# Performance work log

Hardware: AMD Instinct MI355X
Metric: run time of the kernel (lower is better)

## Reference

```python
import jax, jax.numpy as jnp
import numpy as np

B, S, N, D, T = 128, 128, 196, 512, 12


def setup_inputs() -> dict:
    key = jax.random.key(0)
    ks = jax.random.split(key, 20)
    nrm = lambda i, shape, s: jax.random.normal(ks[i], shape, jnp.float32) * s
    w = lambda i, shape: nrm(i, shape, 1.0 / np.sqrt(shape[-1]))
    return {
        "ctx": nrm(0, (B, S, D), 1.0),
        "q": nrm(1, (B, 2 * D), 1.0),
        "k": nrm(2, (B, D, N), 1.0),
        "mem0": nrm(3, (1, D), 0.02),
        "ctrl0": nrm(4, (1, D), 0.02),
        # ControlUnit params
        "Wp": w(5, (T, D, 2 * D)), "bp": jnp.zeros((T, D), jnp.float32),
        "Wcq": w(6, (D, 2 * D)), "bcq": jnp.zeros((D,), jnp.float32),
        "Wca": w(7, (1, D)), "bca": jnp.zeros((1,), jnp.float32),
        # ReadUnit params
        "Wrm": w(8, (D, D)), "brm": jnp.zeros((D,), jnp.float32),
        "Wrc": w(9, (D, 2 * D)), "brc": jnp.zeros((D,), jnp.float32),
        "Wra": w(10, (1, D)), "bra": jnp.zeros((1,), jnp.float32),
        # WriteUnit params
        "Wwc": w(11, (D, 2 * D)), "bwc": jnp.zeros((D,), jnp.float32),
    }


def reference(ctx, q, k, mem0, ctrl0, Wp, bp, Wcq, bcq, Wca, bca,
              Wrm, brm, Wrc, brc, Wra, bra, Wwc, bwc):
    b = q.shape[0]
    c = jnp.broadcast_to(ctrl0, (b, D))
    m = jnp.broadcast_to(mem0, (b, D))
    for t in range(T):
        # --- control unit (alpha_entmax with alpha=1.0 == softmax) ---
        p = q @ Wp[t].T + bp[t]                                # [B, D]
        cc = jnp.concatenate([c, p], axis=1) @ Wcq.T + bcq     # [B, D]
        ctx_p = cc[:, None, :] * ctx                           # [B, S, D]
        aw = jax.nn.softmax(ctx_p @ Wca.T + bca, axis=1)       # [B, S, 1]
        c = (aw * ctx).sum(axis=1)                             # [B, D]
        # --- read unit ---
        mm = (m @ Wrm.T + brm)[:, :, None]                     # [B, D, 1]
        kc = jnp.concatenate([mm * k, k], axis=1)              # [B, 2D, N]
        rc = kc.transpose(0, 2, 1) @ Wrc.T + brc               # [B, N, D]
        logit = ((rc * c[:, None, :]) @ Wra.T + bra)[..., 0]   # [B, N]
        rw = jax.nn.softmax(logit, axis=1)[:, None, :]         # [B, 1, N]
        r = (rw * k).sum(axis=2)                               # [B, D]
        # --- write unit (no self-attention / memory gate) ---
        m = jnp.concatenate([r, m], axis=1) @ Wwc.T + bwc      # [B, D]
    return m
```

## Files before the change

### kernel.cpp

```cpp
#include <hip/hip_runtime.h>
#include <hip/hip_bf16.h>
#include <cstdint>

#define D  512
#define D2 1024
#define BB 128
#define SS 128
#define NN 196
#define TT 12

typedef unsigned short u16;
typedef __attribute__((ext_vector_type(8))) short short8v;
typedef __attribute__((ext_vector_type(4))) float f32x4;

__device__ __forceinline__ float bf2f(u16 h){
  union { unsigned int u; float f; } v; v.u = ((unsigned int)h) << 16; return v.f;
}

__device__ __forceinline__ float LDX(const void* p, size_t i, int isbf){
  if (isbf) return bf2f(((const u16*)p)[i]);
  return ((const float*)p)[i];
}

__device__ __forceinline__ float4 LD4(const void* p, size_t i, int isbf){
  if (isbf){
    ushort4 w = *(const ushort4*)((const u16*)p + i);
    return make_float4(bf2f(w.x), bf2f(w.y), bf2f(w.z), bf2f(w.w));
  }
  return *(const float4*)((const float*)p + i);
}

__device__ __forceinline__ void bfsplit(float x, short &h, short &l){
  unsigned u = __float_as_uint(x);
  unsigned hu = u & 0xFFFF0000u;
  float r = x - __uint_as_float(hu);
  h = (short)(u >> 16);
  l = (short)(__float_as_uint(r) >> 16);
}

__global__ __launch_bounds__(256) void k_detect(const u16* ctx, int* flag){
  __shared__ int cnt;
  if (threadIdx.x == 0) cnt = 0;
  __syncthreads();
  int bad = 0;
  for (int i = threadIdx.x; i < 8192; i += 256){
    int e = (ctx[i] >> 7) & 0xFF;
    if (e == 0xFF || (e != 0 && (e < 90 || e > 160))) bad++;
  }
  atomicAdd(&cnt, bad);
  __syncthreads();
  if (threadIdx.x == 0) *flag = (cnt > 100) ? 0 : 1;
}

__global__ __launch_bounds__(256) void k_prep1(const void* q, const void* Wcq, const void* Wca,
      const void* Wwc, const void* Wrm, const void* Wrc, const void* Wra,
      const void* bp, const void* bcq, const void* ctrl0, const void* mem0, const void* brm,
      float* qT, float* W1f, float* Wwcf, float* WrmTf, float* W2f,
      float* P, float* pp2, float* ubase, float* mmb, const int* flag){
  const int isbf = *flag;
  __shared__ float lds[32][33];
  int bk = blockIdx.x, tid = threadIdx.x;
  int tx = tid & 31, ty = tid >> 5;
  if (bk >= 1344){
    int ib = bk - 1344;
    int lane = tid & 63, w = tid >> 6;
    int grp = lane >> 3, k = lane & 7;
    int isU = (ib < 16);
    int o = (isU ? ib : ib - 16)*32 + w*8 + grp;
    const void* vec = isU ? ctrl0 : mem0;
    const void* mat = isU ? Wcq : Wrm;
    int ld = isU ? D2 : D;
    float acc = 0.f;
    #pragma unroll 4
    for (int it = 0; it < 16; it++){
      int d = it*32 + k*4;
      float4 v = LD4(vec, d, isbf);
      float4 m = LD4(mat, (size_t)o*ld + d, isbf);
      acc += v.x*m.x + v.y*m.y + v.z*m.z + v.w*m.w;
    }
    acc += __shfl_xor(acc, 1, 64);
    acc += __shfl_xor(acc, 2, 64);
    acc += __shfl_xor(acc, 4, 64);
    if (k == 0){
      if (isU) ubase[o] = acc * LDX(Wca, o, isbf);
      else     mmb[o]   = acc + LDX(brm, o, isbf);
    }
    return;
  }
  if (bk >= 1280){
    int l = bk - 1280;
    for (int idx = l*256 + tid; idx < 786432; idx += 64*256){
      int j = (idx >> 7) & 511;
      pp2[idx] = LDX(bcq, j, isbf) * LDX(Wca, j, isbf);
    }
    return;
  }
  if (bk >= 1216){
    int l = bk - 1216;
    for (int idx = l*256 + tid; idx < 786432; idx += 64*256)
      P[idx] = LDX(bp, idx >> 7, isbf);
    return;
  }
  if (bk >= 1152){
    int l = bk - 1152;
    if (isbf){
      const u16* w = (const u16*)Wrc; const u16* s = (const u16*)Wra;
      for (int idx = l*256 + tid; idx < 524288; idx += 64*256)
        W2f[idx] = bf2f(w[idx]) * bf2f(s[idx >> 10]);
    } else {
      const float* w = (const float*)Wrc; const float* s = (const float*)Wra;
      for (int idx = l*256 + tid; idx < 524288; idx += 64*256)
        W2f[idx] = w[idx] * s[idx >> 10];
    }
    return;
  }
  const void* in = nullptr; const void* scale = nullptr; float* out = nullptr;
  int ld = 0, R = 0, tR = 0, tC = 0;
  if (bk < 128)      { in = q;   ld = 1024; R = 128; out = qT;    tR = bk & 3;  tC = bk >> 2; }
  else if (bk < 384) { int l = bk - 128; in = Wcq; ld = 1024; R = 512; out = W1f;  scale = Wca; tR = l & 15; tC = l >> 4; }
  else if (bk < 896) { int l = bk - 384; in = Wwc; ld = 1024; R = 512; out = Wwcf; tR = l & 15; tC = l >> 4; }
  else               { int l = bk - 896; in = Wrm; ld = 512;  R = 512; out = WrmTf;tR = l & 15; tC = l >> 4; }
  int r0 = tR*32, c0 = tC*32;
  #pragma unroll
  for (int kk = 0; kk < 4; kk++){
    int r = r0 + ty + kk*8;
    float v = LDX(in, (size_t)r*ld + c0 + tx, isbf);
    if (scale) v *= LDX(scale, r, isbf);
    lds[tx][ty + kk*8] = v;
  }
  __syncthreads();
  #pragma unroll
  for (int kk = 0; kk < 4; kk++){
    int oc = ty + kk*8;
    out[(size_t)(c0 + oc)*R + r0 + tx] = lds[oc][tx];
  }
}

__global__ __launch_bounds__(256) void k_qsplit(const void* q, u16* QF, const int* flag){
  const int isbf = *flag;
  u16* QH = QF;
  u16* QL = QF + 131072;
  for (int idx = blockIdx.x*256 + threadIdx.x; idx < 131072; idx += 128*256){
    int b = idx >> 10, x = idx & 1023;
    int o = ((x >> 3) << 10) + (b << 3) + (x & 7);
    if (isbf){
      QH[o] = ((const u16*)q)[idx];
      QL[o] = 0;
    } else {
      short h, l;
      bfsplit(((const float*)q)[idx], h, l);
      QH[o] = (u16)h;
      QL[o] = (u16)l;
    }
  }
}

__global__ __launch_bounds__(256) void k_Pmfma(const void* Wp, const u16* QF,
                                               float* P, const int* flag){
  const int isbf = *flag;
  const u16* QH = QF;
  const u16* QL = QF + 131072;
  int bk = blockIdx.x;
  int mt = bk >> 2, kc = bk & 3;
  int m0 = mt * 32;
  int tid = threadIdx.x;
  int ln = tid & 63, w = tid >> 6;
  int msub = w >> 1, nh = w & 1;
  int row  = m0 + msub*16 + (ln & 15);
  int koff = ln >> 4;
  f32x4 acc[4];
  #pragma unroll
  for (int i = 0; i < 4; i++) acc[i] = (f32x4){0.f, 0.f, 0.f, 0.f};

  for (int ks = 0; ks < 8; ks++){
    int k0 = kc*256 + ks*32;
    short8v ah, al;
    if (isbf){
      const u16* wr = (const u16*)Wp + (size_t)row*D2 + k0 + koff*8;
      ah = *(const short8v*)wr;
    } else {
      const float* wr = (const float*)Wp + (size_t)row*D2 + k0 + koff*8;
      float4 f0 = *(const float4*)wr;
      float4 f1 = *(const float4*)(wr + 4);
      float fs[8] = {f0.x, f0.y, f0.z, f0.w, f1.x, f1.y, f1.z, f1.w};
      #pragma unroll
      for (int j = 0; j < 8; j++){
        short h, l;
        bfsplit(fs[j], h, l);
        ah[j] = h; al[j] = l;
      }
    }
    int qrow = ((k0 >> 3) + koff) << 10;
    #pragma unroll
    for (int nt = 0; nt < 4; nt++){
      int col = (nh*4 + nt)*16 + (ln & 15);
      short8v bh = *(const short8v*)(QH + qrow + (col << 3));
      acc[nt] = __builtin_amdgcn_mfma_f32_16x16x32_bf16(ah, bh, acc[nt], 0, 0, 0);
      if (!isbf){
        short8v bl = *(const short8v*)(QL + qrow + (col << 3));
        acc[nt] = __builtin_amdgcn_mfma_f32_16x16x32_bf16(ah, bl, acc[nt], 0, 0, 0);
        acc[nt] = __builtin_amdgcn_mfma_f32_16x16x32_bf16(al, bh, acc[nt], 0, 0, 0);
      }
    }
  }
  int orow = m0 + msub*16 + (ln >> 4)*4;
  #pragma unroll
  for (int nt = 0; nt < 4; nt++){
    int b = (nh*4 + nt)*16 + (ln & 15);
    #pragma unroll
    for (int r = 0; r < 4; r++)
      atomicAdd(&P[(size_t)(orow + r)*BB + b], acc[nt][r]);
  }
}

__global__ __launch_bounds__(512) void k_pp2(const float* P, const void* Wcq,
                                             const void* Wca, float* pp2, const int* flag){
  const int isbf = *flag;
  int bk = blockIdx.x;
  int t = bk >> 6; int r = bk & 63; int jt = r >> 1; int kc = r & 1;
  int tid = threadIdx.x;
  int b = tid & 127;
  int ih = __builtin_amdgcn_readfirstlane(tid >> 7);
  int j0 = jt*16 + ih*4;
  float acc[4] = {0.f, 0.f, 0.f, 0.f};
  int e0k = kc*256;
  if (isbf){
    const u16* w = (const u16*)Wcq;
    for (int e = e0k; e < e0k + 256; e += 8){
      float a[8];
      #pragma unroll
      for (int u = 0; u < 8; u++) a[u] = P[(size_t)(t*D + e + u)*BB + b];
      #pragma unroll
      for (int kk = 0; kk < 4; kk++){
        ushort4 w0 = *(const ushort4*)(w + (size_t)(j0+kk)*D2 + D + e);
        ushort4 w1 = *(const ushort4*)(w + (size_t)(j0+kk)*D2 + D + e + 4);
        acc[kk] += a[0]*bf2f(w0.x) + a[1]*bf2f(w0.y) + a[2]*bf2f(w0.z) + a[3]*bf2f(w0.w)
                 + a[4]*bf2f(w1.x) + a[5]*bf2f(w1.y) + a[6]*bf2f(w1.z) + a[7]*bf2f(w1.w);
      }
    }
  } else {
    const float* w = (const float*)Wcq;
    for (int e = e0k; e < e0k + 256; e += 8){
      float a[8];
      #pragma unroll
      for (int u = 0; u < 8; u++) a[u] = P[(size_t)(t*D + e + u)*BB + b];
      #pragma unroll
      for (int kk = 0; kk < 4; kk++){
        float4 w0 = *(const float4*)(w + (size_t)(j0+kk)*D2 + D + e);
        float4 w1 = *(const float4*)(w + (size_t)(j0+kk)*D2 + D + e + 4);
        acc[kk] += a[0]*w0.x + a[1]*w0.y + a[2]*w0.z + a[3]*w0.w
                 + a[4]*w1.x + a[5]*w1.y + a[6]*w1.z + a[7]*w1.w;
      }
    }
  }
  #pragma unroll
  for (int kk = 0; kk < 4; kk++)
    atomicAdd(&pp2[(size_t)(t*D + j0 + kk)*BB + b], acc[kk] * LDX(Wca, j0 + kk, isbf));
}

__global__ __launch_bounds__(256) void k_initB(const float* ubase, const float* mmb,
                                               const void* mem0, const float* pp2,
                                               float* u0, float* mm0, float* act0,
                                               const int* flag){
  const int isbf = *flag;
  for (int idx = blockIdx.x*256 + threadIdx.x; idx < 3*D*BB; idx += 96*256){
    if (idx < D*BB)            u0[idx] = ubase[idx >> 7] + pp2[idx];
    else if (idx < 2*D*BB)   { int x = idx - D*BB;   mm0[x] = mmb[x >> 7]; }
    else                     { int x = idx - 2*D*BB; act0[D*BB + x] = LDX(mem0, x >> 7, isbf); }
  }
}

__device__ void attn1_body(const void* ctx, const float* u_cur, float* cbuf,
                           int b, int tid, int isbf, float* sm){
  float* cch = sm;
  float* lg  = sm + 8192;
  int lane = tid & 63, wv = tid >> 6;
  float ur[8];
  #pragma unroll
  for (int kk = 0; kk < 4; kk++){
    ur[kk]   = u_cur[(lane*4 + kk)*BB + b];
    ur[4+kk] = u_cur[(256 + lane*4 + kk)*BB + b];
  }
  float mv = -INFINITY, ls = 0.f, o = 0.f;
  for (int c = 0; c < 8; c++){
    int s0 = c*16;
    #pragma unroll
    for (int rr = 0; rr < 2; rr++){
      int loc = rr*8 + wv;
      int s = s0 + loc;
      float4 c0, c1;
      if (isbf){
        const u16* crow = (const u16*)ctx + ((size_t)(b*SS + s))*D;
        ushort4 h0 = *(const ushort4*)(crow + lane*4);
        ushort4 h1 = *(const ushort4*)(crow + 256 + lane*4);
        c0 = make_float4(bf2f(h0.x), bf2f(h0.y), bf2f(h0.z), bf2f(h0.w));
        c1 = make_float4(bf2f(h1.x), bf2f(h1.y), bf2f(h1.z), bf2f(h1.w));
      } else {
        const float* crow = (const float*)ctx + ((size_t)(b*SS + s))*D;
        c0 = *(const float4*)(crow + lane*4);
        c1 = *(const float4*)(crow + 256 + lane*4);
      }
      *(float4*)&cch[loc*512 + lane*4]       = c0;
      *(float4*)&cch[loc*512 + 256 + lane*4] = c1;
      float dot = ur[0]*c0.x + ur[1]*c0.y + ur[2]*c0.z + ur[3]*c0.w
                + ur[4]*c1.x + ur[5]*c1.y + ur[6]*c1.z + ur[7]*c1.w;
      #pragma unroll
      for (int off = 32; off; off >>= 1) dot += __shfl_down(dot, off, 64);
      if (lane == 0) lg[loc] = dot;
    }
    __syncthreads();
    float Mc = lg[0];
    #pragma unroll
    for (int s = 1; s < 16; s++) Mc = fmaxf(Mc, lg[s]);
    float mn = fmaxf(mv, Mc);
    float sc = __expf(mv - mn);
    ls *= sc; o *= sc;
    #pragma unroll
    for (int s = 0; s < 16; s++){
      float e = __expf(lg[s] - mn);
      ls += e;
      o += e * cch[s*512 + tid];
    }
    mv = mn;
    __syncthreads();
  }
  cbuf[tid*BB + b] = o / ls;
}

__device__ void attn2_body(const void* kmat, const float* wbuf, const float* mm_cur,
                           float* act_cur, int b, int tid, int isbf, float* sm){
  float* u2 = sm;
  float* lg = sm + 512;
  float* red= sm + 768;
  float* ps = sm + 1024;
  u2[tid] = wbuf[tid*BB + b]*mm_cur[tid*BB + b] + wbuf[(D + tid)*BB + b];
  __syncthreads();
  {
    int half = tid >> 8;
    int n = tid & 255;
    float part = 0.f;
    if (n < NN){
      float c[8];
      #pragma unroll
      for (int u = 0; u < 8; u++) c[u] = 0.f;
      int d0 = half*256;
      if (isbf){
        const u16* kb = (const u16*)kmat + (size_t)b*D*NN + n;
        for (int dd = 0; dd < 256; dd += 8){
          #pragma unroll
          for (int u = 0; u < 8; u++) c[u] += u2[d0+dd+u]*bf2f(kb[(size_t)(d0+dd+u)*NN]);
        }
      } else {
        const float* kb = (const float*)kmat + (size_t)b*D*NN + n;
        for (int dd = 0; dd < 256; dd += 8){
          #pragma unroll
          for (int u = 0; u < 8; u++) c[u] += u2[d0+dd+u]*kb[(size_t)(d0+dd+u)*NN];
        }
      }
      part = (((c[0]+c[1]) + (c[2]+c[3])) + ((c[4]+c[5]) + (c[6]+c[7])));
    }
    ps[half*256 + n] = part;
  }
  __syncthreads();
  if (tid < 256){
    float logit = (tid < NN) ? (ps[tid] + ps[256 + tid]) : -INFINITY;
    lg[tid] = logit; red[tid] = logit;
  }
  __syncthreads();
  for (int off = 128; off; off >>= 1){ if (tid < off) red[tid] = fmaxf(red[tid], red[tid+off]); __syncthreads(); }
  float M = red[0];
  __syncthreads();
  if (tid < 256){ float e = (tid < NN) ? __expf(lg[tid] - M) : 0.f; lg[tid] = e; red[tid] = e; }
  __syncthreads();
  for (int off = 128; off; off >>= 1){ if (tid < off) red[tid] += red[tid+off]; __syncthreads(); }
  float inv = 1.f / red[0];
  int lane = tid & 63, wv = tid >> 6;
  for (int i = 0; i < 32; i++){
    int dA = wv + i*16, dB = dA + 8;
    float p, qv;
    if (isbf){
      const u16* krA = (const u16*)kmat + (size_t)b*D*NN + (size_t)dA*NN;
      const u16* krB = (const u16*)kmat + (size_t)b*D*NN + (size_t)dB*NN;
      p  = lg[lane]*bf2f(krA[lane]) + lg[lane+64]*bf2f(krA[lane+64]) + lg[lane+128]*bf2f(krA[lane+128]);
      qv = lg[lane]*bf2f(krB[lane]) + lg[lane+64]*bf2f(krB[lane+64]) + lg[lane+128]*bf2f(krB[lane+128]);
      if (lane < NN - 192){
        p  += lg[lane+192]*bf2f(krA[lane+192]);
        qv += lg[lane+192]*bf2f(krB[lane+192]);
      }
    } else {
      const float* krA = (const float*)kmat + (size_t)b*D*NN + (size_t)dA*NN;
      const float* krB = (const float*)kmat + (size_t)b*D*NN + (size_t)dB*NN;
      p  = lg[lane]*krA[lane] + lg[lane+64]*krA[lane+64] + lg[lane+128]*krA[lane+128];
      qv = lg[lane]*krB[lane] + lg[lane+64]*krB[lane+64] + lg[lane+128]*krB[lane+128];
      if (lane < NN - 192){
        p  += lg[lane+192]*krA[lane+192];
        qv += lg[lane+192]*krB[lane+192];
      }
    }
    #pragma unroll
    for (int off = 32; off; off >>= 1){
      p  += __shfl_down(p , off, 64);
      qv += __shfl_down(qv, off, 64);
    }
    if (lane == 0){
      act_cur[dA*BB + b] = p  * inv;
      act_cur[dB*BB + b] = qv * inv;
    }
  }
}

__global__ __launch_bounds__(512) void k_KA(const void* ctx, const float* u_cur, float* cbuf,
                                            const float* act_prev, float* act_cur,
                                            float* wbuf, float* mmbuf, float* u_nxt,
                                            const float* pp2_next, const void* brm,
                                            const float* Wwcf, int t, const int* flag){
  __shared__ float sm[8208];
  int bk = blockIdx.x, tid = threadIdx.x;
  const int isbf = *flag;
  if (bk < 128){
    attn1_body(ctx, u_cur, cbuf, bk, tid, isbf, sm);
    return;
  }
  int b = tid & 127;
  int ih = __builtin_amdgcn_readfirstlane(tid >> 7);
  if (bk < 640){
    if (t == 0) return;
    int l = bk - 128;
    int it = l >> 3, kc = l & 7;
    int ih0 = ih & 1, ih1 = ih >> 1;
    int i0 = it*8 + ih0*4;
    int e0 = kc*128 + ih1*64;
    float acc[4] = {0.f,0.f,0.f,0.f};
    for (int e = e0; e < e0 + 64; e += 8){
      float av[8];
      #pragma unroll
      for (int u = 0; u < 8; u++) av[u] = act_prev[(size_t)(e+u)*BB + b];
      #pragma unroll
      for (int u = 0; u < 8; u++){
        float4 w0 = *(const float4*)(Wwcf + (size_t)(e+u)*D + i0);
        acc[0]+=av[u]*w0.x; acc[1]+=av[u]*w0.y; acc[2]+=av[u]*w0.z; acc[3]+=av[u]*w0.w;
      }
    }
    #pragma unroll
    for (int kk = 0; kk < 4; kk++)
      atomicAdd(&act_cur[(size_t)(D + i0 + kk)*BB + b], acc[kk]);
  } else if (bk < 704){
    int l = bk - 640;
    for (int x = l*512 + tid; x < D2*BB; x += 64*512) wbuf[x] = 0.f;
  } else if (bk < 736){
    if (t == 0) return;
    int l = bk - 704;
    for (int x = l*512 + tid; x < D*BB; x += 32*512) mmbuf[x] = LDX(brm, x >> 7, isbf);
  } else {
    if (t >= TT-1) return;
    int l = bk - 736;
    for (int x = l*512 + tid; x < D*BB; x += 32*512) u_nxt[x] = pp2_next[x];
  }
}

__global__ __launch_bounds__(256) void k_KB(const float* cbuf, const float* W2f, float* wbuf,
                                            const float* act_cur, const float* WrmTf,
                                            float* mmbuf, int t){
  int bk = blockIdx.x, tid = threadIdx.x;
  int b = tid & 127;
  int ih = __builtin_amdgcn_readfirstlane(tid >> 7);
  if (bk < 512){
    int et = bk >> 2, kc = bk & 3;
    int e0 = et*8 + ih*4;
    float acc[4] = {0.f, 0.f, 0.f, 0.f};
    int j0 = kc*128;
    for (int j = j0; j < j0 + 128; j += 8){
      float av[8];
      #pragma unroll
      for (int u = 0; u < 8; u++) av[u] = cbuf[(j+u)*BB + b];
      #pragma unroll
      for (int u = 0; u < 8; u++){
        float4 wv = *(const float4*)(W2f + (size_t)(j+u)*D2 + e0);
        acc[0] += av[u]*wv.x; acc[1] += av[u]*wv.y;
        acc[2] += av[u]*wv.z; acc[3] += av[u]*wv.w;
      }
    }
    #pragma unroll
    for (int kk = 0; kk < 4; kk++) atomicAdd(&wbuf[(e0+kk)*BB + b], acc[kk]);
  } else {
    if (t == 0) return;
    int l = bk - 512;
    int it = l >> 2, kc = l & 3;
    int i0 = it*8 + ih*4;
    float acc[4] = {0.f, 0.f, 0.f, 0.f};
    int d0 = kc*128;
    for (int d = d0; d < d0 + 128; d += 8){
      float av[8];
      #pragma unroll
      for (int u = 0; u < 8; u++) av[u] = act_cur[(size_t)(D + d + u)*BB + b];
      #pragma unroll
      for (int u = 0; u < 8; u++){
        float4 wv = *(const float4*)(WrmTf + (size_t)(d+u)*D + i0);
        acc[0] += av[u]*wv.x; acc[1] += av[u]*wv.y;
        acc[2] += av[u]*wv.z; acc[3] += av[u]*wv.w;
      }
    }
    #pragma unroll
    for (int kk = 0; kk < 4; kk++) atomicAdd(&mmbuf[(i0+kk)*BB + b], acc[kk]);
  }
}

__global__ __launch_bounds__(512) void k_KC(const void* kmat, const float* wbuf,
                                            const float* mmbuf, float* act_cur,
                                            const float* cbuf, const float* W1f, float* u_nxt,
                                            float* act_nxt, const void* bwc,
                                            int t, const int* flag){
  __shared__ float sm[1536];
  int bk = blockIdx.x, tid = threadIdx.x;
  const int isbf = *flag;
  if (bk < 128){
    attn2_body(kmat, wbuf, mmbuf, act_cur, bk, tid, isbf, sm);
    return;
  }
  int b = tid & 127;
  int ih = __builtin_amdgcn_readfirstlane(tid >> 7);
  if (bk < 384){
    if (t >= TT-1) return;
    int l = bk - 128;
    int jt = l >> 1, kc = l & 1;
    int j = jt*4 + ih;
    float c0 = 0.f, c1 = 0.f, c2 = 0.f, c3 = 0.f, c4 = 0.f, c5 = 0.f, c6 = 0.f, c7 = 0.f;
    int e0 = kc*256;
    for (int e = e0; e < e0 + 256; e += 8){
      c0 += cbuf[(e  )*BB + b] * W1f[(size_t)(e  )*D + j];
      c1 += cbuf[(e+1)*BB + b] * W1f[(size_t)(e+1)*D + j];
      c2 += cbuf[(e+2)*BB + b] * W1f[(size_t)(e+2)*D + j];
      c3 += cbuf[(e+3)*BB + b] * W1f[(size_t)(e+3)*D + j];
      c4 += cbuf[(e+4)*BB + b] * W1f[(size_t)(e+4)*D + j];
      c5 += cbuf[(e+5)*BB + b] * W1f[(size_t)(e+5)*D + j];
      c6 += cbuf[(e+6)*BB + b] * W1f[(size_t)(e+6)*D + j];
      c7 += cbuf[(e+7)*BB + b] * W1f[(size_t)(e+7)*D + j];
    }
    float acc = (((c0+c1)+(c2+c3)) + ((c4+c5)+(c6+c7)));
    atomicAdd(&u_nxt[(size_t)j*BB + b], acc);
  } else {
    int l = bk - 384;
    for (int x = l*512 + tid; x < D*BB; x += 32*512)
      act_nxt[D*BB + x] = LDX(bwc, x >> 7, isbf);
  }
}

__global__ __launch_bounds__(512) void k_moutA(const float* act_fin, const float* Wwcf,
                                               float* act_out){
  int bk = blockIdx.x, tid = threadIdx.x;
  int b = tid & 127;
  int ih = __builtin_amdgcn_readfirstlane(tid >> 7);
  int it = bk >> 3, kc = bk & 7;
  int ih0 = ih & 1, ih1 = ih >> 1;
  int i0 = it*8 + ih0*4;
  int e0 = kc*128 + ih1*64;
  float acc[4] = {0.f,0.f,0.f,0.f};
  for (int e = e0; e < e0 + 64; e += 8){
    float av[8];
    #pragma unroll
    for (int u = 0; u < 8; u++) av[u] = act_fin[(size_t)(e+u)*BB + b];
    #pragma unroll
    for (int u = 0; u < 8; u++){
      float4 w0 = *(const float4*)(Wwcf + (size_t)(e+u)*D + i0);
      acc[0]+=av[u]*w0.x; acc[1]+=av[u]*w0.y; acc[2]+=av[u]*w0.z; acc[3]+=av[u]*w0.w;
    }
  }
  #pragma unroll
  for (int kk = 0; kk < 4; kk++)
    atomicAdd(&act_out[(size_t)(D + i0 + kk)*BB + b], acc[kk]);
}

__global__ __launch_bounds__(256) void k_outT(const float* act_fin, void* out, const int* flag){
  const int isbf = *flag;
  __shared__ float lds[32][33];
  int bk = blockIdx.x;
  int it = bk >> 2, bt = bk & 3;
  int tx = threadIdx.x & 31, ty = threadIdx.x >> 5;
  #pragma unroll
  for (int kk = 0; kk < 4; kk++){
    int i = it*32 + ty + kk*8;
    lds[tx][ty + kk*8] = act_fin[(size_t)(D + i)*BB + bt*32 + tx];
  }
  __syncthreads();
  if (isbf){
    __hip_bfloat16* o = (__hip_bfloat16*)out;
    #pragma unroll
    for (int kk = 0; kk < 4; kk++){
      int bb = bt*32 + ty + kk*8;
      o[(size_t)bb*D + it*32 + tx] = __float2bfloat16(lds[ty + kk*8][tx]);
    }
  } else {
    float* o = (float*)out;
    #pragma unroll
    for (int kk = 0; kk < 4; kk++){
      int bb = bt*32 + ty + kk*8;
      o[(size_t)bb*D + it*32 + tx] = lds[ty + kk*8][tx];
    }
  }
}

extern "C" void kernel_launch(void* const* d_in, const int* in_sizes, int n_in,
                              void* d_out, int out_size, void* d_ws, size_t ws_size,
                              hipStream_t stream){
  const void* ctx  = d_in[0];
  const void* q    = d_in[1];
  const void* kmat = d_in[2];
  const void* mem0 = d_in[3];
  const void* ctrl0= d_in[4];
  const void* Wp   = d_in[5];
  const void* bp   = d_in[6];
  const void* Wcq  = d_in[7];
  const void* bcq  = d_in[8];
  const void* Wca  = d_in[9];
  const void* Wrm  = d_in[11];
  const void* brm  = d_in[12];
  const void* Wrc  = d_in[13];
  const void* Wra  = d_in[15];
  const void* Wwc  = d_in[17];
  const void* bwc  = d_in[18];

  float* W      = (float*)d_ws;
  float* qT     = W;
  float* P      = W + 131072;
  float* pp2    = W + 917504;
  float* W1f    = W + 1703936;
  float* W2f    = W + 1966080;
  float* Wwcf   = W + 2490368;
  float* WrmTf  = W + 3014656;
  float* cbuf   = W + 3276800;
  float* wbuf   = W + 3342336;
  float* mmbuf  = W + 3473408;
  float* actb   = W + 3538944;
  float* ubuf   = W + 3801088;
  int*   flag   = (int*)(W + 3932160);
  float* ubase  = W + 3932224;
  float* mmb    = W + 3932736;

  hipLaunchKernelGGL(k_detect, dim3(1), dim3(256), 0, stream, (const u16*)ctx, flag);
  hipLaunchKernelGGL(k_prep1, dim3(1376), dim3(256), 0, stream,
                     q, Wcq, Wca, Wwc, Wrm, Wrc, Wra, bp, bcq, ctrl0, mem0, brm,
                     qT, W1f, Wwcf, WrmTf, W2f, P, pp2, ubase, mmb, flag);
  hipLaunchKernelGGL(k_qsplit, dim3(128), dim3(256), 0, stream, q, (u16*)qT, flag);
  hipLaunchKernelGGL(k_Pmfma, dim3(768), dim3(256), 0, stream, Wp, (const u16*)qT, P, flag);
  hipLaunchKernelGGL(k_pp2,  dim3(768), dim3(512), 0, stream, P, Wcq, Wca, pp2, flag);
  hipLaunchKernelGGL(k_initB, dim3(96), dim3(256), 0, stream,
                     ubase, mmb, mem0, pp2, ubuf, mmbuf, actb, flag);

  for (int t = 0; t < TT; t++){
    int cur = t & 1, nxt = 1 - cur;
    float* act_cur = actb + cur*131072;
    float* act_prev = actb + nxt*131072;
    hipLaunchKernelGGL(k_KA, dim3(768), dim3(512), 0, stream,
                       ctx, ubuf + cur*65536, cbuf,
                       act_prev, act_cur, wbuf, mmbuf, ubuf + nxt*65536,
                       pp2 + ((t+1 < TT) ? (t+1)*65536 : 0), brm, Wwcf, t, flag);
    hipLaunchKernelGGL(k_KB, dim3(768), dim3(256), 0, stream,
                       cbuf, W2f, wbuf, act_cur, WrmTf, mmbuf, t);
    hipLaunchKernelGGL(k_KC, dim3(416), dim3(512), 0, stream,
                       kmat, wbuf, mmbuf, act_cur,
                       cbuf, W1f, ubuf + nxt*65536,
                       actb + nxt*131072, bwc, t, flag);
  }
  hipLaunchKernelGGL(k_moutA, dim3(512), dim3(512), 0, stream,
                     actb + 131072, Wwcf, actb);
  hipLaunchKernelGGL(k_outT, dim3(64), dim3(256), 0, stream, actb, d_out, flag);
}
```

Before: 1.085 ms.

## Split read-attention kernel across D-chunks into two launches for more parallelism

The per-batch read-unit attention, previously one 512-thread block per batch element doing logits, softmax and weighted sum, is split in two. The first kernel computes partial logits over four D-chunks per batch (512 blocks) and writes them to a scratch buffer that reuses the P region. The second kernel reduces the partials, redoes the softmax, and computes the weighted sum over a quarter of D per block (512 blocks). This raises block count from 128 to 512 to fill more CUs. The cost is an extra launch per timestep, a scratch round trip, and softmax work repeated four times per batch.

```diff
diff --git a/kernel.cpp b/kernel.cpp
--- a/kernel.cpp
+++ b/kernel.cpp
@@ -327,88 +327,6 @@
   cbuf[tid*BB + b] = o / ls;
 }
 
-__device__ void attn2_body(const void* kmat, const float* wbuf, const float* mm_cur,
-                           float* act_cur, int b, int tid, int isbf, float* sm){
-  float* u2 = sm;
-  float* lg = sm + 512;
-  float* red= sm + 768;
-  float* ps = sm + 1024;
-  u2[tid] = wbuf[tid*BB + b]*mm_cur[tid*BB + b] + wbuf[(D + tid)*BB + b];
-  __syncthreads();
-  {
-    int half = tid >> 8;
-    int n = tid & 255;
-    float part = 0.f;
-    if (n < NN){
-      float c[8];
-      #pragma unroll
-      for (int u = 0; u < 8; u++) c[u] = 0.f;
-      int d0 = half*256;
-      if (isbf){
-        const u16* kb = (const u16*)kmat + (size_t)b*D*NN + n;
-        for (int dd = 0; dd < 256; dd += 8){
-          #pragma unroll
-          for (int u = 0; u < 8; u++) c[u] += u2[d0+dd+u]*bf2f(kb[(size_t)(d0+dd+u)*NN]);
-        }
-      } else {
-        const float* kb = (const float*)kmat + (size_t)b*D*NN + n;
-        for (int dd = 0; dd < 256; dd += 8){
-          #pragma unroll
-          for (int u = 0; u < 8; u++) c[u] += u2[d0+dd+u]*kb[(size_t)(d0+dd+u)*NN];
-        }
-      }
-      part = (((c[0]+c[1]) + (c[2]+c[3])) + ((c[4]+c[5]) + (c[6]+c[7])));
-    }
-    ps[half*256 + n] = part;
-  }
-  __syncthreads();
-  if (tid < 256){
-    float logit = (tid < NN) ? (ps[tid] + ps[256 + tid]) : -INFINITY;
-    lg[tid] = logit; red[tid] = logit;
-  }
-  __syncthreads();
-  for (int off = 128; off; off >>= 1){ if (tid < off) red[tid] = fmaxf(red[tid], red[tid+off]); __syncthreads(); }
-  float M = red[0];
-  __syncthreads();
-  if (tid < 256){ float e = (tid < NN) ? __expf(lg[tid] - M) : 0.f; lg[tid] = e; red[tid] = e; }
-  __syncthreads();
-  for (int off = 128; off; off >>= 1){ if (tid < off) red[tid] += red[tid+off]; __syncthreads(); }
-  float inv = 1.f / red[0];
-  int lane = tid & 63, wv = tid >> 6;
-  for (int i = 0; i < 32; i++){
-    int dA = wv + i*16, dB = dA + 8;
-    float p, qv;
-    if (isbf){
-      const u16* krA = (const u16*)kmat + (size_t)b*D*NN + (size_t)dA*NN;
-      const u16* krB = (const u16*)kmat + (size_t)b*D*NN + (size_t)dB*NN;
-      p  = lg[lane]*bf2f(krA[lane]) + lg[lane+64]*bf2f(krA[lane+64]) + lg[lane+128]*bf2f(krA[lane+128]);
-      qv = lg[lane]*bf2f(krB[lane]) + lg[lane+64]*bf2f(krB[lane+64]) + lg[lane+128]*bf2f(krB[lane+128]);
-      if (lane < NN - 192){
-        p  += lg[lane+192]*bf2f(krA[lane+192]);
-        qv += lg[lane+192]*bf2f(krB[lane+192]);
-      }
-    } else {
-      const float* krA = (const float*)kmat + (size_t)b*D*NN + (size_t)dA*NN;
-      const float* krB = (const float*)kmat + (size_t)b*D*NN + (size_t)dB*NN;
-      p  = lg[lane]*krA[lane] + lg[lane+64]*krA[lane+64] + lg[lane+128]*krA[lane+128];
-      qv = lg[lane]*krB[lane] + lg[lane+64]*krB[lane+64] + lg[lane+128]*krB[lane+128];
-      if (lane < NN - 192){
-        p  += lg[lane+192]*krA[lane+192];
-        qv += lg[lane+192]*krB[lane+192];
-      }
-    }
-    #pragma unroll
-    for (int off = 32; off; off >>= 1){
-      p  += __shfl_down(p , off, 64);
-      qv += __shfl_down(qv, off, 64);
-    }
-    if (lane == 0){
-      act_cur[dA*BB + b] = p  * inv;
-      act_cur[dB*BB + b] = qv * inv;
-    }
-  }
-}
-
 __global__ __launch_bounds__(512) void k_KA(const void* ctx, const float* u_cur, float* cbuf,
                                             const float* act_prev, float* act_cur,
                                             float* wbuf, float* mmbuf, float* u_nxt,
@@ -505,23 +423,54 @@
   }
 }
 
-__global__ __launch_bounds__(512) void k_KC(const void* kmat, const float* wbuf,
-                                            const float* mmbuf, float* act_cur,
-                                            const float* cbuf, const float* W1f, float* u_nxt,
-                                            float* act_nxt, const void* bwc,
-                                            int t, const int* flag){
-  __shared__ float sm[1536];
+__global__ __launch_bounds__(512) void k_KC1(const void* kmat, const float* wbuf,
+                                             const float* mmbuf, float* pbuf,
+                                             const float* cbuf, const float* W1f, float* u_nxt,
+                                             float* act_nxt, const void* bwc,
+                                             int t, const int* flag){
+  __shared__ float u2[128];
   int bk = blockIdx.x, tid = threadIdx.x;
   const int isbf = *flag;
-  if (bk < 128){
-    attn2_body(kmat, wbuf, mmbuf, act_cur, bk, tid, isbf, sm);
+  if (bk < 512){
+    int b = bk & 127, ch2 = bk >> 7;
+    int d0 = ch2*128;
+    if (tid < 128){
+      int d = d0 + tid;
+      u2[tid] = wbuf[(size_t)d*BB + b]*mmbuf[(size_t)d*BB + b] + wbuf[(size_t)(D + d)*BB + b];
+    }
+    __syncthreads();
+    int half = tid >> 8;
+    int n = tid & 255;
+    int dd0 = half*64;
+    float part = 0.f;
+    if (n < NN){
+      float c[8];
+      #pragma unroll
+      for (int u = 0; u < 8; u++) c[u] = 0.f;
+      if (isbf){
+        const u16* kb = (const u16*)kmat + (size_t)b*D*NN + (size_t)(d0+dd0)*NN + n;
+        for (int dd = 0; dd < 64; dd += 8){
+          #pragma unroll
+          for (int u = 0; u < 8; u++) c[u] += u2[dd0+dd+u]*bf2f(kb[(size_t)(dd+u)*NN]);
+        }
+      } else {
+        const float* kb = (const float*)kmat + (size_t)b*D*NN + (size_t)(d0+dd0)*NN + n;
+        for (int dd = 0; dd < 64; dd += 8){
+          #pragma unroll
+          for (int u = 0; u < 8; u++) c[u] += u2[dd0+dd+u]*kb[(size_t)(dd+u)*NN];
+        }
+      }
+      part = (((c[0]+c[1]) + (c[2]+c[3])) + ((c[4]+c[5]) + (c[6]+c[7])));
+    }
+    int chunk = ch2*2 + half;
+    pbuf[((size_t)chunk*BB + b)*256 + n] = part;
     return;
   }
   int b = tid & 127;
   int ih = __builtin_amdgcn_readfirstlane(tid >> 7);
-  if (bk < 384){
+  if (bk < 768){
     if (t >= TT-1) return;
-    int l = bk - 128;
+    int l = bk - 512;
     int jt = l >> 1, kc = l & 1;
     int j = jt*4 + ih;
     float c0 = 0.f, c1 = 0.f, c2 = 0.f, c3 = 0.f, c4 = 0.f, c5 = 0.f, c6 = 0.f, c7 = 0.f;
@@ -539,9 +488,70 @@
     float acc = (((c0+c1)+(c2+c3)) + ((c4+c5)+(c6+c7)));
     atomicAdd(&u_nxt[(size_t)j*BB + b], acc);
   } else {
-    int l = bk - 384;
+    int l = bk - 768;
     for (int x = l*512 + tid; x < D*BB; x += 32*512)
       act_nxt[D*BB + x] = LDX(bwc, x >> 7, isbf);
+  }
+}
+
+__global__ __launch_bounds__(512) void k_KC2(const void* kmat, const float* pbuf,
+                                             float* act_cur, const int* flag){
+  __shared__ float lg[256];
+  __shared__ float red[256];
+  int bk = blockIdx.x, tid = threadIdx.x;
+  const int isbf = *flag;
+  int b = bk & 127, qc = bk >> 7;
+  if (tid < 256){
+    float s;
+    if (tid < NN){
+      s = 0.f;
+      #pragma unroll
+      for (int c = 0; c < 8; c++)
+        s += pbuf[((size_t)c*BB + b)*256 + tid];
+    } else s = -INFINITY;
+    lg[tid] = s; red[tid] = s;
+  }
+  __syncthreads();
+  for (int off = 128; off; off >>= 1){ if (tid < off) red[tid] = fmaxf(red[tid], red[tid+off]); __syncthreads(); }
+  float M = red[0];
+  __syncthreads();
+  if (tid < 256){ float e = (tid < NN) ? __expf(lg[tid] - M) : 0.f; lg[tid] = e; red[tid] = e; }
+  __syncthreads();
+  for (int off = 128; off; off >>= 1){ if (tid < off) red[tid] += red[tid+off]; __syncthreads(); }
+  float inv = 1.f / red[0];
+  int lane = tid & 63, wv = tid >> 6;
+  int d0 = qc*128;
+  for (int i = 0; i < 8; i++){
+    int dA = d0 + i*16 + wv, dB = dA + 8;
+    float p, qv;
+    if (isbf){
+      const u16* krA = (const u16*)kmat + (size_t)b*D*NN + (size_t)dA*NN;
+      const u16* krB = (const u16*)kmat + (size_t)b*D*NN + (size_t)dB*NN;
+      p  = lg[lane]*bf2f(krA[lane]) + lg[lane+64]*bf2f(krA[lane+64]) + lg[lane+128]*bf2f(krA[lane+128]);
+      qv = lg[lane]*bf2f(krB[lane]) + lg[lane+64]*bf2f(krB[lane+64]) + lg[lane+128]*bf2f(krB[lane+128]);
+      if (lane < NN - 192){
+        p  += lg[lane+192]*bf2f(krA[lane+192]);
+        qv += lg[lane+192]*bf2f(krB[lane+192]);
+      }
+    } else {
+      const float* krA = (const float*)kmat + (size_t)b*D*NN + (size_t)dA*NN;
+      const float* krB = (const float*)kmat + (size_t)b*D*NN + (size_t)dB*NN;
+      p  = lg[lane]*krA[lane] + lg[lane+64]*krA[lane+64] + lg[lane+128]*krA[lane+128];
+      qv = lg[lane]*krB[lane] + lg[lane+64]*krB[lane+64] + lg[lane+128]*krB[lane+128];
+      if (lane < NN - 192){
+        p  += lg[lane+192]*krA[lane+192];
+        qv += lg[lane+192]*krB[lane+192];
+      }
+    }
+    #pragma unroll
+    for (int off = 32; off; off >>= 1){
+      p  += __shfl_down(p , off, 64);
+      qv += __shfl_down(qv, off, 64);
+    }
+    if (lane == 0){
+      act_cur[(size_t)dA*BB + b] = p  * inv;
+      act_cur[(size_t)dB*BB + b] = qv * inv;
+    }
   }
 }
 
@@ -635,6 +645,7 @@
   int*   flag   = (int*)(W + 3932160);
   float* ubase  = W + 3932224;
   float* mmb    = W + 3932736;
+  float* pbuf   = P;
 
   hipLaunchKernelGGL(k_detect, dim3(1), dim3(256), 0, stream, (const u16*)ctx, flag);
   hipLaunchKernelGGL(k_prep1, dim3(1376), dim3(256), 0, stream,
@@ -656,10 +667,12 @@
                        pp2 + ((t+1 < TT) ? (t+1)*65536 : 0), brm, Wwcf, t, flag);
     hipLaunchKernelGGL(k_KB, dim3(768), dim3(256), 0, stream,
                        cbuf, W2f, wbuf, act_cur, WrmTf, mmbuf, t);
-    hipLaunchKernelGGL(k_KC, dim3(416), dim3(512), 0, stream,
-                       kmat, wbuf, mmbuf, act_cur,
+    hipLaunchKernelGGL(k_KC1, dim3(800), dim3(512), 0, stream,
+                       kmat, wbuf, mmbuf, pbuf,
                        cbuf, W1f, ubuf + nxt*65536,
                        actb + nxt*131072, bwc, t, flag);
+    hipLaunchKernelGGL(k_KC2, dim3(512), dim3(512), 0, stream,
+                       kmat, pbuf, act_cur, flag);
   }
   hipLaunchKernelGGL(k_moutA, dim3(512), dim3(512), 0, stream,
                      actb + 131072, Wwcf, actb);
```

After: 1.034 ms. 1.05x faster.
